# Kernel optimization log

Hardware: AMD Instinct MI355X
Metric: run time of the kernel (lower is better)

Reference implementation:

```python
import jax, jax.numpy as jnp
import numpy as np

T, B, D, H, R, O = 32, 8, 512, 512, 32, 512
CLIP_VAL = 1.0
LN_EPS = 1e-5


def setup_inputs() -> dict:
    key = jax.random.key(0)
    ks = jax.random.split(key, 8)
    rn = lambda k, sh, sc: (jax.random.normal(k, sh) * sc).astype(jnp.float32)
    inp = {
        'x': rn(ks[0], (T, B, D), 1.0),
        'h0': jnp.zeros((B, H), jnp.float32),
        'v0': jnp.zeros((B, H), jnp.float32),
        'dU0': jnp.zeros((B, H, H), jnp.float32),
        'trace_e0': jnp.zeros((B, H), jnp.float32),
        'trace_E0': jnp.zeros((B, H, H), jnp.float32),
        # parameters (init-scale approximations of the torch inits)
        'x2h_w': rn(ks[1], (2 * H, D), 1.0 / np.sqrt(D)),
        'x2h_b': jnp.zeros((2 * H,), jnp.float32),
        'h2h_w': rn(ks[2], (2 * H, H), 1.0 / np.sqrt(H)),
        'h2h_b': jnp.zeros((2 * H,), jnp.float32),
        'lnx_g': jnp.ones((2 * H,), jnp.float32),
        'lnx_b': jnp.zeros((2 * H,), jnp.float32),
        'lnh_g': jnp.ones((2 * H,), jnp.float32),
        'lnh_b': jnp.zeros((2 * H,), jnp.float32),
        'h2mod_w': rn(ks[3], (R, H), np.sqrt(2.0 / H)),
        'h2mod_b': jnp.zeros((R,), jnp.float32),
        'mod2h_w': rn(ks[4], (3, R), np.sqrt(2.0 / R)),
        'mod2h_b': jnp.zeros((3,), jnp.float32),
        'alpha': jnp.full((1,), -4.0, jnp.float32),
        'tau_U': jnp.full((1,), -4.5, jnp.float32),
        'dec_w': rn(ks[5], (O, H), 1.0 / np.sqrt(H)),
        'dec_b': jnp.zeros((O,), jnp.float32),
    }
    return inp


def _ln(y, g, b):
    mu = jnp.mean(y, axis=-1, keepdims=True)
    yc = y - mu
    var = jnp.mean(yc * yc, axis=-1, keepdims=True)
    return g * yc * jax.lax.rsqrt(var + LN_EPS) + b


def reference(x, h0, v0, dU0, trace_e0, trace_E0,
              x2h_w, x2h_b, h2h_w, h2h_b,
              lnx_g, lnx_b, lnh_g, lnh_b,
              h2mod_w, h2mod_b, mod2h_w, mod2h_b,
              alpha, tau_U, dec_w, dec_b):
    Hh = h0.shape[-1]
    sp_alpha = jax.nn.softplus(alpha)            # (1,)
    tau = jax.nn.sigmoid(tau_U)                  # (1,)
    # clip bounds derived from the candidate-row block of h2h weight
    w_dv = h2h_w[Hh:2 * Hh]                      # [H, H]
    upper = jax.nn.relu(CLIP_VAL - w_dv) / (sp_alpha + 1e-8)
    lower = -jax.nn.relu(CLIP_VAL + w_dv) / (sp_alpha + 1e-8)

    def step(carry, xt):
        h, v, dU, te, tE = carry
        Wx = _ln(xt @ x2h_w.T + x2h_b, lnx_g, lnx_b)           # [B, 2H]
        Wh = h @ h2h_w.T + h2h_b                               # [B, 2H]
        plast = sp_alpha * jnp.einsum('bij,bj->bi', dU, h)     # [B, H]
        Wh = Wh.at[:, Hh:].add(plast)
        Wh = _ln(Wh, lnh_g, lnh_b)
        z, dv = jnp.split(Wx + Wh, 2, axis=-1)
        z = jax.nn.sigmoid(z)
        v_n = (1.0 - z) * v + z * dv
        nh = jax.nn.relu(v_n)
        mod = jax.nn.relu(nh @ h2mod_w.T + h2mod_b) @ mod2h_w.T + mod2h_b  # [B, 3]
        r = jax.nn.sigmoid(mod[:, :1])                          # [B, 1]
        s = jax.nn.sigmoid(mod[:, 1])[:, None, None]            # [B, 1, 1]
        m = mod[:, 2][:, None, None]                            # [B, 1, 1]
        te_n = (1.0 - r) * te + r * h
        outer = nh[:, :, None] * te_n[:, None, :]               # [B, H, H]
        tE_n = (1.0 - s) * tE + s * (outer - jnp.swapaxes(outer, 1, 2))
        dU_n = (1.0 - tau) * dU + tau * m * tE_n
        dU_n = jnp.where(dU_n > upper, upper, dU_n)
        dU_n = jnp.where(dU_n < lower, lower, dU_n)
        return (nh, v_n, dU_n, te_n, tE_n), nh

    carry0 = (h0, v0, dU0, trace_e0, trace_E0)
    _, hs = jax.lax.scan(step, carry0, x)                        # hs: [T, B, H]
    out = hs @ dec_w.T + dec_b                                   # [T, B, O]
    return out
```

## Files before the change

kernel.cpp:

```cpp
#include <hip/hip_runtime.h>

#define TT 32
#define BB 8
#define DD 512
#define HH 512
#define RR 32
#define OO 512
#define H2 1024

typedef unsigned int uint;

#define OFF_WX    0
#define OFF_COLV  393216
#define OFF_FLAGS 409600

#define AGENT __HIP_MEMORY_SCOPE_AGENT
#define RLX   __ATOMIC_RELAXED

#define HMW_P 528

__device__ __forceinline__ void st_coh(float* p, float v) {
  __hip_atomic_store(p, v, RLX, AGENT);
}
__device__ __forceinline__ float ld_coh(const float* p) {
  return __hip_atomic_load(const_cast<float*>(p), RLX, AGENT);
}
__device__ __forceinline__ float d4(const float4& a, const float4& b) {
  return a.x*b.x + a.y*b.y + a.z*b.z + a.w*b.w;
}

__device__ __forceinline__ void bar32(unsigned* flags, int b, int ir,
                                      unsigned seq, int tid) {
  __syncthreads();
  asm volatile("s_waitcnt vmcnt(0)" ::: "memory");
  if (tid == 0)
    __hip_atomic_store(&flags[b*32 + ir], seq, RLX, AGENT);
  if (tid < 64) {
    for (;;) {
      unsigned v = (tid < 32) ? __hip_atomic_load(&flags[b*32 + tid], RLX, AGENT) : seq;
      if (__all(v >= seq)) break;
      __builtin_amdgcn_s_sleep(1);
    }
  }
  __syncthreads();
}

template<bool UPDATE>
__device__ __forceinline__ void gemv_step(
    int gi, int m,
    float4 (&dUr)[4], float4 (&tEr)[4],
    const float4 (&Wdvr)[4], const float4 (&wlo)[4],
    const float4 (&upr)[4], const float4 (&lor)[4],
    float s_b, float c1t, float c2t, float a_sp, float hbl, float hbh,
    const float* nh_s, const float* te_s,
    float* post)
{
  const float nh_i = nh_s[gi];
  const float te_i = UPDATE ? te_s[gi] : 0.0f;
  const float4* nh4 = reinterpret_cast<const float4*>(nh_s);
  const float4* te4 = reinterpret_cast<const float4*>(te_s);
  float plast = 0.0f, gdv = 0.0f, glo = 0.0f;
#pragma unroll
  for (int q = 0; q < 4; ++q) {
    const int J = m + 32*q;
    const float4 h4 = nh4[J];
    if (UPDATE) {
      const float4 t4 = te4[J];
#define SGRU_UPD(C) { \
      float o   = nh_i * t4.C - h4.C * te_i;                 \
      float tEn = tEr[q].C + s_b * (o - tEr[q].C);           \
      tEr[q].C  = tEn;                                                               \
      float d   = c1t * dUr[q].C + c2t * tEn;                \
      d = fminf(d, upr[q].C); d = fmaxf(d, lor[q].C);        \
      dUr[q].C  = d;                                                                 \
      plast = fmaf(d, h4.C, plast); }
      SGRU_UPD(x) SGRU_UPD(y) SGRU_UPD(z) SGRU_UPD(w)
#undef SGRU_UPD
    } else {
      plast += d4(dUr[q], h4);
    }
    gdv += d4(Wdvr[q], h4);
    glo += d4(wlo[q],  h4);
  }
#pragma unroll
  for (int off = 16; off >= 1; off >>= 1) {
    plast += __shfl_xor(plast, off);
    gdv   += __shfl_xor(gdv, off);
    glo   += __shfl_xor(glo, off);
  }
  if (m == 0) {
    st_coh(&post[gi],      glo + hbl);
    st_coh(&post[HH + gi], gdv + hbh + a_sp * plast);
  }
}

__global__ __launch_bounds__(512, 1) void sgru_persistent(
    const float* __restrict__ h0,     const float* __restrict__ v0,
    const float* __restrict__ dU0,    const float* __restrict__ tE0,
    const float* __restrict__ te0,
    const float* __restrict__ h2h_w,  const float* __restrict__ h2h_b,
    const float* __restrict__ lnh_g,  const float* __restrict__ lnh_b,
    const float* __restrict__ h2mod_w,const float* __restrict__ h2mod_b,
    const float* __restrict__ mod2h_w,const float* __restrict__ mod2h_b,
    const float* __restrict__ alpha_p,const float* __restrict__ tau_p,
    const float* __restrict__ dec_w,  const float* __restrict__ dec_b,
    float* __restrict__ out,          float* __restrict__ ws)
{
  const int tid = threadIdx.x;
  const int b   = blockIdx.x & 7;
  const int ir  = blockIdx.x >> 3;
  const int i0  = ir << 4;
  const int il  = tid >> 5;
  const int m   = tid & 31;
  const int gi  = i0 + il;

  const float* Wx = ws + OFF_WX;
  float* colvG    = ws + OFF_COLV;
  unsigned* flags = (unsigned*)(ws + OFF_FLAGS);

  __shared__ float nh_s[2][HH];
  __shared__ float te_s[HH];
  __shared__ float hmw_s[RR * HMW_P];
  __shared__ float mp_s[RR];
  __shared__ float rsm_s[4];
  __shared__ float red_s[2][8];

  const float a_sp  = log1pf(__expf(alpha_p[0]));
  const float inv_a = 1.0f / (a_sp + 1e-8f);
  const float tau   = 1.0f / (1.0f + __expf(-tau_p[0]));
  const float c1t   = 1.0f - tau;

  float4 dUr[4], tEr[4], Wdvr[4], wlo[4], upr[4], lor[4];
  {
    const size_t rowoff = ((size_t)b * HH + gi) * HH;
    const size_t whioff = (size_t)(HH + gi) * HH;
    const size_t wlooff = (size_t)gi * HH;
#pragma unroll
    for (int q = 0; q < 4; ++q) {
      const int J = m + 32*q;
      dUr[q] = *reinterpret_cast<const float4*>(dU0 + rowoff + 4*J);
      tEr[q] = *reinterpret_cast<const float4*>(tE0 + rowoff + 4*J);
      wlo[q] = *reinterpret_cast<const float4*>(h2h_w + wlooff + 4*J);
      const float4 w = *reinterpret_cast<const float4*>(h2h_w + whioff + 4*J);
      Wdvr[q] = w;
      float4 u, l;
      u.x =  fmaxf(1.0f - w.x, 0.0f) * inv_a;  l.x = -fmaxf(1.0f + w.x, 0.0f) * inv_a;
      u.y =  fmaxf(1.0f - w.y, 0.0f) * inv_a;  l.y = -fmaxf(1.0f + w.y, 0.0f) * inv_a;
      u.z =  fmaxf(1.0f - w.z, 0.0f) * inv_a;  l.z = -fmaxf(1.0f + w.z, 0.0f) * inv_a;
      u.w =  fmaxf(1.0f - w.w, 0.0f) * inv_a;  l.w = -fmaxf(1.0f + w.w, 0.0f) * inv_a;
      upr[q] = u; lor[q] = l;
    }
  }

  const float rgz = lnh_g[tid],      rbz = lnh_b[tid];
  const float rgd = lnh_g[HH + tid], rbd = lnh_b[HH + tid];
  const float hbl = h2h_b[gi], hbh = h2h_b[HH + gi];
  const float hmb = h2mod_b[tid >> 4];
  const float mw0 = (tid < RR) ? mod2h_w[tid]        : 0.0f;
  const float mw1 = (tid < RR) ? mod2h_w[RR + tid]   : 0.0f;
  const float mw2 = (tid < RR) ? mod2h_w[2*RR + tid] : 0.0f;
  const float mb0 = mod2h_b[0], mb1 = mod2h_b[1], mb2 = mod2h_b[2];
  const float dbc = dec_b[gi];
  const float* drow = dec_w + (size_t)gi * HH;
  float vreg = v0[b*HH + tid];

  nh_s[1][tid] = h0[b*HH + tid];
  te_s[tid]    = te0[b*HH + tid];
  for (int idx = tid; idx < RR*HH; idx += 512)
    hmw_s[(idx >> 9)*HMW_P + (idx & 511)] = h2mod_w[idx];
  __syncthreads();

  gemv_step<false>(gi, m, dUr, tEr, Wdvr, wlo, upr, lor,
                   0.0f, c1t, 0.0f, a_sp, hbl, hbh,
                   nh_s[1], te_s, colvG + 0*BB*H2 + b*H2);

  float wxz = Wx[(size_t)(0*BB + b)*H2 + tid];
  float wxd = Wx[(size_t)(0*BB + b)*H2 + HH + tid];

  unsigned seq = 0;
  for (int t = 0; t < TT; ++t) {
    const int cur = t & 1;
    bar32(flags, b, ir, ++seq, tid);

    const float whz = ld_coh(&colvG[cur*BB*H2 + b*H2 + tid]);
    const float whd = ld_coh(&colvG[cur*BB*H2 + b*H2 + HH + tid]);

    float s1 = whz + whd, s2 = whz*whz + whd*whd;
#pragma unroll
    for (int off = 32; off >= 1; off >>= 1) {
      s1 += __shfl_xor(s1, off);
      s2 += __shfl_xor(s2, off);
    }
    if ((tid & 63) == 0) { red_s[0][tid >> 6] = s1; red_s[1][tid >> 6] = s2; }
    __syncthreads();
    s1 = 0.0f; s2 = 0.0f;
#pragma unroll
    for (int w = 0; w < 8; ++w) { s1 += red_s[0][w]; s2 += red_s[1][w]; }
    const float mu   = s1 * (1.0f / H2);
    const float var  = s2 * (1.0f / H2) - mu * mu;
    const float rstd = rsqrtf(var + 1e-5f);

    const float yz = (whz - mu)*rstd*rgz + rbz + wxz;
    const float yd = (whd - mu)*rstd*rgd + rbd + wxd;
    const float z  = 1.0f / (1.0f + __expf(-yz));
    vreg = vreg + z * (yd - vreg);
    const float nh = fmaxf(vreg, 0.0f);
    nh_s[cur][tid] = nh;

    if (t == TT - 1) {
      __syncthreads();
      const float4* nh4 = reinterpret_cast<const float4*>(nh_s[cur]);
      float acc = 0.0f;
#pragma unroll
      for (int q = 0; q < 4; ++q) {
        const int J = m + 32*q;
        acc += d4(*reinterpret_cast<const float4*>(drow + 4*J), nh4[J]);
      }
#pragma unroll
      for (int off = 16; off >= 1; off >>= 1) acc += __shfl_xor(acc, off);
      if (m == 0) out[(size_t)(t*BB + b)*OO + gi] = acc + dbc;
      return;
    }

    wxz = Wx[(size_t)((t+1)*BB + b)*H2 + tid];
    wxd = Wx[(size_t)((t+1)*BB + b)*H2 + HH + tid];
    __syncthreads();

    {
      const int r = tid >> 4, kk = tid & 15;
      float part = 0.0f;
#pragma unroll
      for (int j = 0; j < 32; ++j)
        part += hmw_s[r*HMW_P + kk + 16*j] * nh_s[cur][kk + 16*j];
#pragma unroll
      for (int off = 8; off >= 1; off >>= 1) part += __shfl_xor(part, off);
      if (kk == 0) mp_s[r] = fmaxf(part + hmb, 0.0f);
    }
    __syncthreads();
    if (tid < 64) {
      const float mp = (tid < RR) ? mp_s[tid] : 0.0f;
      float a0 = mw0*mp, a1 = mw1*mp, a2 = mw2*mp;
#pragma unroll
      for (int off = 16; off >= 1; off >>= 1) {
        a0 += __shfl_xor(a0, off);
        a1 += __shfl_xor(a1, off);
        a2 += __shfl_xor(a2, off);
      }
      if (tid == 0) {
        rsm_s[0] = 1.0f / (1.0f + __expf(-(a0 + mb0)));
        rsm_s[1] = 1.0f / (1.0f + __expf(-(a1 + mb1)));
        rsm_s[2] = a2 + mb2;
      }
    }
    __syncthreads();
    const float r_b = rsm_s[0];
    const float s_b = rsm_s[1];
    const float c2t = tau * rsm_s[2];

    te_s[tid] += r_b * (nh_s[1 - cur][tid] - te_s[tid]);
    __syncthreads();

    gemv_step<true>(gi, m, dUr, tEr, Wdvr, wlo, upr, lor,
                    s_b, c1t, c2t, a_sp, hbl, hbh,
                    nh_s[cur], te_s, colvG + (1 - cur)*BB*H2 + b*H2);

    {
      const float4* nh4 = reinterpret_cast<const float4*>(nh_s[cur]);
      float acc = 0.0f;
#pragma unroll
      for (int q = 0; q < 4; ++q) {
        const int J = m + 32*q;
        acc += d4(*reinterpret_cast<const float4*>(drow + 4*J), nh4[J]);
      }
#pragma unroll
      for (int off = 16; off >= 1; off >>= 1) acc += __shfl_xor(acc, off);
      if (m == 0) out[(size_t)(t*BB + b)*OO + gi] = acc + dbc;
    }
  }
}

#define GBM 32
#define GBN 32
#define GBK 32
__global__ __launch_bounds__(256) void gemm_tn(
    const float* __restrict__ A, const float* __restrict__ W,
    const float* __restrict__ bias, float* __restrict__ C,
    int M, int N)
{
  const int K = 512;
  const int nbn = N / GBN;
  const int m0 = (blockIdx.x / nbn) * GBM;
  const int n0 = (blockIdx.x % nbn) * GBN;
  const int tid = threadIdx.x;
  const int tx = tid & 15;
  const int ty = tid >> 4;
  const int lr = tid >> 3;
  const int lc = tid & 7;
  __shared__ float As[GBK][36];
  __shared__ float Ws[GBK][36];
  float acc[2][2] = {};
  for (int kc = 0; kc < K; kc += GBK) {
    const float4 a0 = *reinterpret_cast<const float4*>(A + (size_t)(m0 + lr)*K + kc + lc*4);
    const float4 w0 = *reinterpret_cast<const float4*>(W + (size_t)(n0 + lr)*K + kc + lc*4);
    __syncthreads();
    As[lc*4+0][lr] = a0.x; As[lc*4+1][lr] = a0.y; As[lc*4+2][lr] = a0.z; As[lc*4+3][lr] = a0.w;
    Ws[lc*4+0][lr] = w0.x; Ws[lc*4+1][lr] = w0.y; Ws[lc*4+2][lr] = w0.z; Ws[lc*4+3][lr] = w0.w;
    __syncthreads();
#pragma unroll
    for (int k = 0; k < GBK; ++k) {
      const float2 am = *reinterpret_cast<const float2*>(&As[k][ty*2]);
      const float2 wn = *reinterpret_cast<const float2*>(&Ws[k][tx*2]);
      acc[0][0] += am.x*wn.x; acc[0][1] += am.x*wn.y;
      acc[1][0] += am.y*wn.x; acc[1][1] += am.y*wn.y;
    }
  }
  const float b0 = bias[n0 + tx*2], b1 = bias[n0 + tx*2 + 1];
  C[(size_t)(m0 + ty*2 + 0)*N + n0 + tx*2]     = acc[0][0] + b0;
  C[(size_t)(m0 + ty*2 + 0)*N + n0 + tx*2 + 1] = acc[0][1] + b1;
  C[(size_t)(m0 + ty*2 + 1)*N + n0 + tx*2]     = acc[1][0] + b0;
  C[(size_t)(m0 + ty*2 + 1)*N + n0 + tx*2 + 1] = acc[1][1] + b1;
}

__global__ __launch_bounds__(256) void ln_apply(
    float* __restrict__ Wp, const float* __restrict__ g, const float* __restrict__ b,
    unsigned* __restrict__ flags)
{
  const int row = blockIdx.x;
  const int tid = threadIdx.x;
  if (row == 0) flags[tid] = 0u;
  float* rp = Wp + (size_t)row * H2;
  float4 v = *reinterpret_cast<const float4*>(rp + tid*4);
  float s1 = v.x + v.y + v.z + v.w;
  float s2 = v.x*v.x + v.y*v.y + v.z*v.z + v.w*v.w;
#pragma unroll
  for (int off = 32; off >= 1; off >>= 1) {
    s1 += __shfl_xor(s1, off);
    s2 += __shfl_xor(s2, off);
  }
  __shared__ float red[2][4];
  if ((tid & 63) == 0) { red[0][tid >> 6] = s1; red[1][tid >> 6] = s2; }
  __syncthreads();
  s1 = red[0][0] + red[0][1] + red[0][2] + red[0][3];
  s2 = red[1][0] + red[1][1] + red[1][2] + red[1][3];
  const float mu   = s1 * (1.0f / H2);
  const float var  = s2 * (1.0f / H2) - mu * mu;
  const float rstd = rsqrtf(var + 1e-5f);
  const float4 gv = *reinterpret_cast<const float4*>(g + tid*4);
  const float4 bv = *reinterpret_cast<const float4*>(b + tid*4);
  v.x = gv.x*(v.x - mu)*rstd + bv.x;
  v.y = gv.y*(v.y - mu)*rstd + bv.y;
  v.z = gv.z*(v.z - mu)*rstd + bv.z;
  v.w = gv.w*(v.w - mu)*rstd + bv.w;
  *reinterpret_cast<float4*>(rp + tid*4) = v;
}

extern "C" void kernel_launch(void* const* d_in, const int* in_sizes, int n_in,
                              void* d_out, int out_size, void* d_ws, size_t ws_size,
                              hipStream_t stream) {
  (void)in_sizes; (void)n_in; (void)out_size; (void)ws_size;
  const float* x        = (const float*)d_in[0];
  const float* h0       = (const float*)d_in[1];
  const float* v0       = (const float*)d_in[2];
  const float* dU0      = (const float*)d_in[3];
  const float* te0      = (const float*)d_in[4];
  const float* tE0      = (const float*)d_in[5];
  const float* x2h_w    = (const float*)d_in[6];
  const float* x2h_b    = (const float*)d_in[7];
  const float* h2h_w    = (const float*)d_in[8];
  const float* h2h_b    = (const float*)d_in[9];
  const float* lnx_g    = (const float*)d_in[10];
  const float* lnx_b    = (const float*)d_in[11];
  const float* lnh_g    = (const float*)d_in[12];
  const float* lnh_b    = (const float*)d_in[13];
  const float* h2mod_w  = (const float*)d_in[14];
  const float* h2mod_b  = (const float*)d_in[15];
  const float* mod2h_w  = (const float*)d_in[16];
  const float* mod2h_b  = (const float*)d_in[17];
  const float* alpha    = (const float*)d_in[18];
  const float* tau_U    = (const float*)d_in[19];
  const float* dec_w    = (const float*)d_in[20];
  const float* dec_b    = (const float*)d_in[21];

  float* ws = (float*)d_ws;

  gemm_tn<<<(TT*BB/GBM) * (H2/GBN), 256, 0, stream>>>(x, x2h_w, x2h_b,
                                                      ws + OFF_WX, TT*BB, H2);
  ln_apply<<<TT*BB, 256, 0, stream>>>(ws + OFF_WX, lnx_g, lnx_b,
                                      (unsigned*)(ws + OFF_FLAGS));

  sgru_persistent<<<256, 512, 0, stream>>>(h0, v0, dU0, tE0, te0,
                                           h2h_w, h2h_b, lnh_g, lnh_b,
                                           h2mod_w, h2mod_b, mod2h_w, mod2h_b,
                                           alpha, tau_U, dec_w, dec_b,
                                           (float*)d_out, ws);
}
```

Measured before the change: 177.3 us.

## Overlap decoder projection with inter-block barrier spin and stage dec_w in LDS

The per-step decoder dot products move off the critical path. They now run on waves 1-4 while wave 0 spins on the cross-block flag barrier, computing the previous step's outputs from the other nh buffer. The block's 16 dec_w rows are staged once into padded shared memory instead of being read from global memory every step. This adds about 33KB of LDS and makes the barrier code more complex, and it relies on nh_s[1-cur] not being overwritten before the decode finishes.

```diff
diff --git a/kernel.cpp b/kernel.cpp
--- a/kernel.cpp
+++ b/kernel.cpp
@@ -18,6 +18,7 @@
 #define RLX   __ATOMIC_RELAXED
 
 #define HMW_P 528
+#define DEC_P 520
 
 __device__ __forceinline__ void st_coh(float* p, float v) {
   __hip_atomic_store(p, v, RLX, AGENT);
@@ -29,20 +30,26 @@
   return a.x*b.x + a.y*b.y + a.z*b.z + a.w*b.w;
 }
 
-__device__ __forceinline__ void bar32(unsigned* flags, int b, int ir,
-                                      unsigned seq, int tid) {
-  __syncthreads();
-  asm volatile("s_waitcnt vmcnt(0)" ::: "memory");
-  if (tid == 0)
-    __hip_atomic_store(&flags[b*32 + ir], seq, RLX, AGENT);
-  if (tid < 64) {
-    for (;;) {
-      unsigned v = (tid < 32) ? __hip_atomic_load(&flags[b*32 + tid], RLX, AGENT) : seq;
-      if (__all(v >= seq)) break;
-      __builtin_amdgcn_s_sleep(1);
-    }
-  }
-  __syncthreads();
+__device__ __forceinline__ void decode_rows(
+    int wid, int lane, int i0, int b, int trow,
+    const float* dec_s, const float* nhp, const float* __restrict__ dec_b,
+    float* __restrict__ out)
+{
+  if (wid >= 1 && wid <= 4) {
+    const int r   = (wid - 1)*4 + (lane >> 4);
+    const int l16 = lane & 15;
+    const float4* dr4 = reinterpret_cast<const float4*>(dec_s + r*DEC_P);
+    const float4* nh4 = reinterpret_cast<const float4*>(nhp);
+    float acc = 0.0f;
+#pragma unroll
+    for (int k = 0; k < 8; ++k) {
+      const int J = l16 + 16*k;
+      acc += d4(dr4[J], nh4[J]);
+    }
+#pragma unroll
+    for (int off = 8; off >= 1; off >>= 1) acc += __shfl_xor(acc, off);
+    if (l16 == 0) out[(size_t)(trow*BB + b)*OO + i0 + r] = acc + dec_b[i0 + r];
+  }
 }
 
 template<bool UPDATE>
@@ -106,7 +113,9 @@
     const float* __restrict__ dec_w,  const float* __restrict__ dec_b,
     float* __restrict__ out,          float* __restrict__ ws)
 {
-  const int tid = threadIdx.x;
+  const int tid  = threadIdx.x;
+  const int wid  = tid >> 6;
+  const int lane = tid & 63;
   const int b   = blockIdx.x & 7;
   const int ir  = blockIdx.x >> 3;
   const int i0  = ir << 4;
@@ -121,6 +130,7 @@
   __shared__ float nh_s[2][HH];
   __shared__ float te_s[HH];
   __shared__ float hmw_s[RR * HMW_P];
+  __shared__ float dec_s[16 * DEC_P];
   __shared__ float mp_s[RR];
   __shared__ float rsm_s[4];
   __shared__ float red_s[2][8];
@@ -160,14 +170,14 @@
   const float mw1 = (tid < RR) ? mod2h_w[RR + tid]   : 0.0f;
   const float mw2 = (tid < RR) ? mod2h_w[2*RR + tid] : 0.0f;
   const float mb0 = mod2h_b[0], mb1 = mod2h_b[1], mb2 = mod2h_b[2];
-  const float dbc = dec_b[gi];
-  const float* drow = dec_w + (size_t)gi * HH;
   float vreg = v0[b*HH + tid];
 
   nh_s[1][tid] = h0[b*HH + tid];
   te_s[tid]    = te0[b*HH + tid];
   for (int idx = tid; idx < RR*HH; idx += 512)
     hmw_s[(idx >> 9)*HMW_P + (idx & 511)] = h2mod_w[idx];
+  for (int idx = tid; idx < 16*HH; idx += 512)
+    dec_s[(idx >> 9)*DEC_P + (idx & 511)] = dec_w[(size_t)i0*HH + idx];
   __syncthreads();
 
   gemv_step<false>(gi, m, dUr, tEr, Wdvr, wlo, upr, lor,
@@ -180,7 +190,22 @@
   unsigned seq = 0;
   for (int t = 0; t < TT; ++t) {
     const int cur = t & 1;
-    bar32(flags, b, ir, ++seq, tid);
+    ++seq;
+
+    __syncthreads();
+    asm volatile("s_waitcnt vmcnt(0)" ::: "memory");
+    if (tid == 0)
+      __hip_atomic_store(&flags[b*32 + ir], seq, RLX, AGENT);
+    if (tid < 64) {
+      for (;;) {
+        unsigned v = (tid < 32) ? __hip_atomic_load(&flags[b*32 + tid], RLX, AGENT) : seq;
+        if (__all(v >= seq)) break;
+        __builtin_amdgcn_s_sleep(1);
+      }
+    } else if (t > 0) {
+      decode_rows(wid, lane, i0, b, t - 1, dec_s, nh_s[1 - cur], dec_b, out);
+    }
+    __syncthreads();
 
     const float whz = ld_coh(&colvG[cur*BB*H2 + b*H2 + tid]);
     const float whd = ld_coh(&colvG[cur*BB*H2 + b*H2 + HH + tid]);
@@ -209,16 +234,7 @@
 
     if (t == TT - 1) {
       __syncthreads();
-      const float4* nh4 = reinterpret_cast<const float4*>(nh_s[cur]);
-      float acc = 0.0f;
-#pragma unroll
-      for (int q = 0; q < 4; ++q) {
-        const int J = m + 32*q;
-        acc += d4(*reinterpret_cast<const float4*>(drow + 4*J), nh4[J]);
-      }
-#pragma unroll
-      for (int off = 16; off >= 1; off >>= 1) acc += __shfl_xor(acc, off);
-      if (m == 0) out[(size_t)(t*BB + b)*OO + gi] = acc + dbc;
+      decode_rows(wid, lane, i0, b, t, dec_s, nh_s[cur], dec_b, out);
       return;
     }
 
@@ -263,19 +279,6 @@
     gemv_step<true>(gi, m, dUr, tEr, Wdvr, wlo, upr, lor,
                     s_b, c1t, c2t, a_sp, hbl, hbh,
                     nh_s[cur], te_s, colvG + (1 - cur)*BB*H2 + b*H2);
-
-    {
-      const float4* nh4 = reinterpret_cast<const float4*>(nh_s[cur]);
-      float acc = 0.0f;
-#pragma unroll
-      for (int q = 0; q < 4; ++q) {
-        const int J = m + 32*q;
-        acc += d4(*reinterpret_cast<const float4*>(drow + 4*J), nh4[J]);
-      }
-#pragma unroll
-      for (int off = 16; off >= 1; off >>= 1) acc += __shfl_xor(acc, off);
-      if (m == 0) out[(size_t)(t*BB + b)*OO + gi] = acc + dbc;
-    }
   }
 }
 
```

New measurement: 174.0 us. About the same (-1.9%).
